# Optimization experiments

Hardware: AMD Instinct MI355X
Metric: run time of the kernel (lower is better)

The kernel has to match this reference:

```python
import jax, jax.numpy as jnp
import numpy as np

B, S, RAW, E, H, NH = 2048, 8, 1024, 512, 256, 8
CEIL = 0.9998


def _lstm_dir(x, Wih, Whh, bih, bhh, reverse):
    # x: [B,S,D] -> hs: [B,S,H]; torch gate order i,f,g,o
    xs = jnp.swapaxes(x, 0, 1)  # [S,B,D]
    if reverse:
        xs = xs[::-1]
    pre = jnp.einsum('sbd,gd->sbg', xs, Wih) + bih + bhh  # [S,B,4H]
    h0 = jnp.zeros((x.shape[0], Whh.shape[1]), x.dtype)

    def step(carry, p):
        h, c = carry
        g = p + h @ Whh.T
        i, f, gg, o = jnp.split(g, 4, axis=-1)
        c = jax.nn.sigmoid(f) * c + jax.nn.sigmoid(i) * jnp.tanh(gg)
        h = jax.nn.sigmoid(o) * jnp.tanh(c)
        return (h, c), h

    _, hs = jax.lax.scan(step, (h0, h0), pre)
    if reverse:
        hs = hs[::-1]
    return jnp.swapaxes(hs, 0, 1)


def _bilstm(x, Wih, Whh, bih, bhh):
    # stacked weights: Wih [2,2,4H,512], Whh [2,2,4H,H], biases [2,2,4H]
    for l in range(2):
        fwd = _lstm_dir(x, Wih[l, 0], Whh[l, 0], bih[l, 0], bhh[l, 0], False)
        bwd = _lstm_dir(x, Wih[l, 1], Whh[l, 1], bih[l, 1], bhh[l, 1], True)
        x = jnp.concatenate([fwd, bwd], axis=-1)  # [B,S,2H]
    return x


def _mha(x, Wqkv, bqkv, Wo, bo):
    b, s, e = x.shape
    hd = e // NH
    qkv = x @ Wqkv.T + bqkv
    q, k, v = jnp.split(qkv, 3, axis=-1)
    q = q.reshape(b, s, NH, hd).transpose(0, 2, 1, 3)
    k = k.reshape(b, s, NH, hd).transpose(0, 2, 1, 3)
    v = v.reshape(b, s, NH, hd).transpose(0, 2, 1, 3)
    attn = jax.nn.softmax(jnp.einsum('bhqd,bhkd->bhqk', q, k) / jnp.sqrt(jnp.float32(hd)), axis=-1)
    out = jnp.einsum('bhqk,bhkd->bhqd', attn, v).transpose(0, 2, 1, 3).reshape(b, s, e)
    out = out @ Wo.T + bo
    return out, attn.mean(axis=1)  # torch averages weights over heads -> [B,S,S]


def _mlp2(x, W1, b1, W2, b2):
    return jax.nn.relu(x @ W1.T + b1) @ W2.T + b2


def setup_inputs() -> dict:
    key = jax.random.key(0)
    ks = jax.random.split(key, 32)
    g = lambda k, shp: (0.02 * jax.random.normal(k, shp)).astype(jnp.float32)
    inp = {
        'audio_raw': jax.random.normal(ks[0], (B, S, RAW), jnp.float32),
        'visual_raw': jax.random.normal(ks[1], (B, S, RAW), jnp.float32),
        'Wa1': g(ks[2], (512, 1024)), 'ba1': g(ks[3], (512,)),
        'Wa2': g(ks[4], (256, 512)), 'ba2': g(ks[5], (256,)),
        'Wv1': g(ks[6], (512, 1024)), 'bv1': g(ks[7], (512,)),
        'Wv2': g(ks[8], (256, 512)), 'bv2': g(ks[9], (256,)),
        'Wih': g(ks[10], (2, 2, 4 * H, 512)), 'Whh': g(ks[11], (2, 2, 4 * H, H)),
        'bih': g(ks[12], (2, 2, 4 * H)), 'bhh': g(ks[13], (2, 2, 4 * H)),
        'Wqkv': g(ks[14], (3 * E, E)), 'bqkv': g(ks[15], (3 * E,)),
        'Wo': g(ks[16], (E, E)), 'bo': g(ks[17], (E,)),
        'Wc1': g(ks[18], (256, E + 1)), 'bc1': g(ks[19], (256,)),
        'Wc2': g(ks[20], (1, 256)), 'bc2': g(ks[21], (1,)),
    }
    return inp


def reference(audio_raw, visual_raw, Wa1, ba1, Wa2, ba2, Wv1, bv1, Wv2, bv2,
              Wih, Whh, bih, bhh, Wqkv, bqkv, Wo, bo, Wc1, bc1, Wc2, bc2):
    a = _mlp2(audio_raw, Wa1, ba1, Wa2, ba2)    # [B,S,256]
    v = _mlp2(visual_raw, Wv1, bv1, Wv2, bv2)   # [B,S,256]
    seq = jnp.concatenate([a, v], axis=-1)      # [B,S,512]
    lstm_out = _bilstm(seq, Wih, Whh, bih, bhh)  # [B,S,512]
    attn_out, attn_w = _mha(lstm_out, Wqkv, bqkv, Wo, bo)
    weights = jax.nn.softmax(attn_w.mean(axis=1), axis=-1)          # [B,S]
    summary = jnp.einsum('bse,bs->be', attn_out, weights)           # [B,512]
    curiosity_bonus = jnp.zeros((summary.shape[0], 1), summary.dtype)  # replay buffer empty
    c_in = jnp.concatenate([summary, curiosity_bonus], axis=-1)
    coherence = jax.nn.sigmoid(jax.nn.relu(c_in @ Wc1.T + bc1) @ Wc2.T + bc2)[:, 0]
    coherence = jnp.minimum(coherence, CEIL)  # absolute-ceiling veto clip
    return coherence
```

## Files before the change

### kernel.cpp

```cpp
#include <hip/hip_runtime.h>
#include <hip/hip_bf16.h>


#define ROWS   16384
#define BATCH  2048

typedef __bf16 bf16x8 __attribute__((ext_vector_type(8)));
typedef float  f32x4  __attribute__((ext_vector_type(4)));

typedef __hip_bfloat16 bf16;

#define MB(x) ((size_t)(x) << 20)
static const size_t OFF_WB    = 0;
static const size_t OFF_ABF   = MB(12);
static const size_t OFF_VBF   = MB(44);
static const size_t OFF_M1A   = MB(76);
static const size_t OFF_M1V   = MB(92);
static const size_t OFF_SEQ   = MB(108);
static const size_t OFF_PRE   = MB(124);
static const size_t OFF_LSTM1 = MB(210);
static const size_t OFF_LSTM2 = MB(226);
static const size_t OFF_QKV   = MB(12);
static const size_t OFF_CTX   = MB(108);
static const size_t OFF_AOUT  = MB(12);
static const size_t OFF_COLSUM= MB(242);
static const size_t OFF_WTS   = MB(243);
static const size_t OFF_SUMM  = MB(244);
static const size_t OFF_WC1T  = MB(248);

static const size_t WB_WA1  = 0;
static const size_t WB_WV1  = 524288;
static const size_t WB_WA2  = 1048576;
static const size_t WB_WV2  = 1179648;
static const size_t WB_WIH  = 1310720;
static const size_t WB_WHH  = 3407872;
static const size_t WB_WQKV = 4456448;
static const size_t WB_WO   = 5242880;

struct ConvJobs {
    const float* src[10];
    bf16*        dst[10];
    long long    cum[11];
};

__global__ __launch_bounds__(256) void convert_bf16(ConvJobs jobs, long long total4)
{
    for (long long g = (long long)blockIdx.x * 256 + threadIdx.x; g < total4;
         g += (long long)gridDim.x * 256) {
        int j = 0;
        while (g >= jobs.cum[j + 1]) ++j;
        const long long idx = g - jobs.cum[j];
        const float4 v = ((const float4*)jobs.src[j])[idx];
        union { ushort4 u; bf16 h[4]; } p;
        p.h[0] = __float2bfloat16(v.x);
        p.h[1] = __float2bfloat16(v.y);
        p.h[2] = __float2bfloat16(v.z);
        p.h[3] = __float2bfloat16(v.w);
        ((ushort4*)jobs.dst[j])[idx] = p.u;
    }
}

__device__ __forceinline__ void gload_lds16(const void* g, void* l)
{
    __builtin_amdgcn_global_load_lds(
        (const __attribute__((address_space(1))) unsigned int*)g,
        (__attribute__((address_space(3))) unsigned int*)l, 16, 0, 0);
}

__global__ __launch_bounds__(256) void gemm_mfma(
    const bf16* __restrict__ A, long long sAz,
    const bf16* __restrict__ W, long long sWz,
    const float* __restrict__ b1, long long sb1,
    const float* __restrict__ b2, long long sb2,
    const bf16* __restrict__ D, long long sDz, int ldd,
    float* Cf, long long sCfz,
    bf16* Cb, long long sCbz,
    int M, int N, int K, int ldc, int coloff, int relu)
{
    const int z = blockIdx.z;
    A += (long long)z * sAz;
    W += (long long)z * sWz;
    if (b1) b1 += (long long)z * sb1;
    if (b2) b2 += (long long)z * sb2;
    if (D)  D  += (long long)z * sDz;
    if (Cf) Cf += (long long)z * sCfz;
    if (Cb) Cb += (long long)z * sCbz;

    __shared__ bf16 As[128 * 32];
    __shared__ bf16 Bs[128 * 32];

    const int tid  = threadIdx.x;
    const int wave = tid >> 6;
    const int lane = tid & 63;
    const int wm = wave >> 1;
    const int wn = wave & 1;
    const long long m0 = (long long)blockIdx.x * 128;
    const long long n0 = (long long)blockIdx.y * 128;

    const int srow = tid >> 2;
    const int scol = (tid & 3) * 8;

    f32x4 acc[4][4] = {};

    const bf16* Abase = A + (m0 + srow) * (long long)K + scol;
    const bf16* Wbase = W + (n0 + srow) * (long long)K + scol;
    const long long K64 = (long long)K * 64;

    const int lrow = (lane >> 4) * 8;
    const int frow = lane & 15;

    for (int k0 = 0; k0 < K; k0 += 32) {
        gload_lds16(Abase + k0,        As + tid * 8);
        gload_lds16(Abase + k0 + K64,  As + 2048 + tid * 8);
        gload_lds16(Wbase + k0,        Bs + tid * 8);
        gload_lds16(Wbase + k0 + K64,  Bs + 2048 + tid * 8);
        __syncthreads();

        bf16x8 af[4], bfv[4];
#pragma unroll
        for (int i = 0; i < 4; ++i)
            af[i] = *(const bf16x8*)(As + (wm * 64 + i * 16 + frow) * 32 + lrow);
#pragma unroll
        for (int j = 0; j < 4; ++j)
            bfv[j] = *(const bf16x8*)(Bs + (wn * 64 + j * 16 + frow) * 32 + lrow);
#pragma unroll
        for (int i = 0; i < 4; ++i)
#pragma unroll
            for (int j = 0; j < 4; ++j)
                acc[i][j] = __builtin_amdgcn_mfma_f32_16x16x32_bf16(af[i], bfv[j], acc[i][j], 0, 0, 0);
        __syncthreads();
    }

    const long long mwb = m0 + wm * 64;
    const long long nwb = n0 + wn * 64;
    const int rbase = (lane >> 4) * 4;
    const int lcol = lane & 15;
#pragma unroll
    for (int j = 0; j < 4; ++j) {
        const long long col = nwb + j * 16 + lcol;
        float bias = 0.f;
        if (b1) bias += b1[col];
        if (b2) bias += b2[col];
#pragma unroll
        for (int i = 0; i < 4; ++i) {
            const long long rowb = mwb + i * 16 + rbase;
#pragma unroll
            for (int r = 0; r < 4; ++r) {
                const long long row = rowb + r;
                float v = acc[i][j][r] + bias;
                if (D) v += __bfloat162float(D[row * (long long)ldd + col]);
                if (relu) v = fmaxf(v, 0.f);
                if (Cf) Cf[row * (long long)ldc + coloff + col] = v;
                if (Cb) Cb[row * (long long)ldc + coloff + col] = __float2bfloat16(v);
            }
        }
    }
}

__device__ __forceinline__ float sigf(float x) { return 1.f / (1.f + expf(-x)); }

__global__ __launch_bounds__(512) void lstm_layer(
    const bf16* __restrict__ PRE,
    const bf16* __restrict__ Whh,
    bf16* __restrict__ lout)
{
    __shared__ bf16 Bs[128 * 256];
    __shared__ bf16 Hs[16 * 264];

    float* preact = (float*)Bs;

    const int tid  = threadIdx.x;
    const int wave = tid >> 6;
    const int lane = tid & 63;
    const int frow = lane & 15;
    const int g    = lane >> 4;
    const int rbase = g * 4;

    const int R0  = blockIdx.x * 16;
    const int dir = R0 >> 11;
    const int b0  = R0 & 2047;
    const bf16* Wd   = Whh + (size_t)dir * 1024 * 256;
    const bf16* PREd = PRE + (size_t)dir * 16384 * 1024;

    const int gn = tid & 255;
    const int rh = tid >> 8;

    float c_state[8];
#pragma unroll
    for (int i = 0; i < 8; ++i) c_state[i] = 0.f;

    for (int t = 0; t < 8; ++t) {
        if (t > 0) {
            bf16x8 af[8];
#pragma unroll
            for (int ks = 0; ks < 8; ++ks)
                af[ks] = *(const bf16x8*)(Hs + frow * 264 + ks * 32 + g * 8);

            f32x4 acc[8] = {};
            for (int nb = 0; nb < 8; ++nb) {
                __syncthreads();
                const bf16* src = Wd + (size_t)nb * 128 * 256;
#pragma unroll
                for (int q = 0; q < 8; ++q) {
                    const int t16 = q * 512 + tid;
                    const int row = t16 >> 5;
                    const int cl  = t16 & 31;
                    const int cg  = cl ^ (row & 7);
                    gload_lds16(src + row * 256 + cg * 8, Bs + t16 * 8);
                }
                __syncthreads();
                const int lr = wave * 16 + frow;
#pragma unroll
                for (int ks = 0; ks < 8; ++ks) {
                    const int cgk = ks * 4 + g;
                    const bf16x8 bv = *(const bf16x8*)(Bs + lr * 256 + ((cgk ^ (lr & 7)) * 8));
                    acc[nb] = __builtin_amdgcn_mfma_f32_16x16x32_bf16(af[ks], bv, acc[nb], 0, 0, 0);
                }
            }
            __syncthreads();
#pragma unroll
            for (int nb = 0; nb < 8; ++nb) {
                const int col = nb * 128 + wave * 16 + frow;
#pragma unroll
                for (int r = 0; r < 4; ++r)
                    preact[(rbase + r) * 1024 + col] = acc[nb][r];
            }
            __syncthreads();
        }

        const int te = dir ? (7 - t) : t;
#pragma unroll
        for (int i = 0; i < 8; ++i) {
            const int row = i * 2 + rh;
            const int b = b0 + row;
            const bf16* pr = PREd + ((size_t)b * 8 + te) * 1024;
            float ig = __bfloat162float(pr[gn]);
            float fg = __bfloat162float(pr[gn + 256]);
            float gg = __bfloat162float(pr[gn + 512]);
            float og = __bfloat162float(pr[gn + 768]);
            if (t > 0) {
                ig += preact[row * 1024 + gn];
                fg += preact[row * 1024 + gn + 256];
                gg += preact[row * 1024 + gn + 512];
                og += preact[row * 1024 + gn + 768];
            }
            const float c = sigf(fg) * c_state[i] + sigf(ig) * tanhf(gg);
            const float h = sigf(og) * tanhf(c);
            c_state[i] = c;
            Hs[row * 264 + gn] = __float2bfloat16(h);
            lout[((size_t)b * 8 + te) * 512 + dir * 256 + gn] = __float2bfloat16(h);
        }
        __syncthreads();
    }
}

__global__ __launch_bounds__(64) void attn_kernel(
    const bf16* __restrict__ qkv,
    bf16* __restrict__ ctx,
    float* __restrict__ colsum)
{
    const int bh = blockIdx.x;
    const int b = bh >> 3;
    const int h = bh & 7;
    const int t = threadIdx.x;

    __shared__ float q[8][64], k[8][64], v[8][64], p[8][8];
    const bf16* base = qkv + (size_t)b * 8 * 1536 + h * 64;
#pragma unroll
    for (int s = 0; s < 8; ++s) {
        q[s][t] = __bfloat162float(base[s * 1536 + t]);
        k[s][t] = __bfloat162float(base[s * 1536 + 512 + t]);
        v[s][t] = __bfloat162float(base[s * 1536 + 1024 + t]);
    }
    __syncthreads();

    const int qi = t >> 3;
    const int kj = t & 7;
    float sc = 0.f;
#pragma unroll
    for (int d = 0; d < 64; ++d) sc += q[qi][d] * k[kj][d];
    sc *= 0.125f;

    float mx = sc;
    for (int off = 1; off < 8; off <<= 1) mx = fmaxf(mx, __shfl_xor(mx, off));
    const float e = expf(sc - mx);
    float sum = e;
    for (int off = 1; off < 8; off <<= 1) sum += __shfl_xor(sum, off);
    const float P = e / sum;
    p[qi][kj] = P;

    float cs = P;
    for (int off = 8; off < 64; off <<= 1) cs += __shfl_xor(cs, off);
    if (t < 8) colsum[(size_t)bh * 8 + t] = cs;
    __syncthreads();

    bf16* cb = ctx + ((size_t)b * 8 + qi) * 512 + h * 64;
#pragma unroll
    for (int j = 0; j < 8; ++j) {
        const int d = (t & 7) + 8 * j;
        float o = 0.f;
#pragma unroll
        for (int kk = 0; kk < 8; ++kk) o += p[qi][kk] * v[kk][d];
        cb[d] = __float2bfloat16(o);
    }
}

__global__ __launch_bounds__(64) void weights_kernel(
    const float* __restrict__ colsum, float* __restrict__ wts)
{
    const int t = threadIdx.x;
    const int b = blockIdx.x * 8 + (t >> 3);
    const int kk = t & 7;
    const float* cs = colsum + (size_t)b * 64;
    float s = 0.f;
#pragma unroll
    for (int h = 0; h < 8; ++h) s += cs[h * 8 + kk];
    s *= (1.f / 64.f);
    float mx = s;
    for (int off = 1; off < 8; off <<= 1) mx = fmaxf(mx, __shfl_xor(mx, off));
    const float e = expf(s - mx);
    float sum = e;
    for (int off = 1; off < 8; off <<= 1) sum += __shfl_xor(sum, off);
    wts[(size_t)b * 8 + kk] = e / sum;
}

__global__ __launch_bounds__(256) void summary_kernel(
    const float* __restrict__ aout, const float* __restrict__ wts,
    float* __restrict__ summ)
{
    const int gid = blockIdx.x * 256 + threadIdx.x;
    const int b = gid >> 9;
    const int e = gid & 511;
    const float* ab = aout + (size_t)b * 8 * 512 + e;
    const float* wb = wts + (size_t)b * 8;
    float s = 0.f;
#pragma unroll
    for (int t = 0; t < 8; ++t) s += ab[t * 512] * wb[t];
    summ[gid] = s;
}

__global__ __launch_bounds__(256) void transpose_wc1(
    const float* __restrict__ Wc1, float* __restrict__ Wc1T)
{
    const int gid = blockIdx.x * 256 + threadIdx.x;
    const int j = gid / 513;
    const int e = gid % 513;
    Wc1T[(size_t)e * 256 + j] = Wc1[gid];
}

__global__ __launch_bounds__(256) void coherence_kernel(
    const float* __restrict__ summ, const float* __restrict__ Wc1T,
    const float* __restrict__ bc1, const float* __restrict__ Wc2,
    const float* __restrict__ bc2, float* __restrict__ out)
{
    const int b = blockIdx.x;
    const int j = threadIdx.x;
    __shared__ float s[512];
    __shared__ float red[4];
    s[j]       = summ[(size_t)b * 512 + j];
    s[j + 256] = summ[(size_t)b * 512 + 256 + j];
    __syncthreads();

    float hj = bc1[j];
    for (int e = 0; e < 512; ++e) hj += s[e] * Wc1T[(size_t)e * 256 + j];
    hj = fmaxf(hj, 0.f);
    float val = hj * Wc2[j];
    for (int off = 1; off < 64; off <<= 1) val += __shfl_xor(val, off);
    if ((j & 63) == 0) red[j >> 6] = val;
    __syncthreads();
    if (j == 0) {
        const float tot = red[0] + red[1] + red[2] + red[3] + bc2[0];
        const float c = 1.f / (1.f + expf(-tot));
        out[b] = fminf(c, 0.9998f);
    }
}

extern "C" void kernel_launch(void* const* d_in, const int* in_sizes, int n_in,
                              void* d_out, int out_size, void* d_ws, size_t ws_size,
                              hipStream_t stream)
{
    (void)in_sizes; (void)n_in; (void)out_size; (void)ws_size;

    const float* audio  = (const float*)d_in[0];
    const float* visual = (const float*)d_in[1];
    const float* Wa1 = (const float*)d_in[2];  const float* ba1 = (const float*)d_in[3];
    const float* Wa2 = (const float*)d_in[4];  const float* ba2 = (const float*)d_in[5];
    const float* Wv1 = (const float*)d_in[6];  const float* bv1 = (const float*)d_in[7];
    const float* Wv2 = (const float*)d_in[8];  const float* bv2 = (const float*)d_in[9];
    const float* Wih = (const float*)d_in[10]; const float* Whh = (const float*)d_in[11];
    const float* bih = (const float*)d_in[12]; const float* bhh = (const float*)d_in[13];
    const float* Wqkv = (const float*)d_in[14]; const float* bqkv = (const float*)d_in[15];
    const float* Wo  = (const float*)d_in[16]; const float* bo  = (const float*)d_in[17];
    const float* Wc1 = (const float*)d_in[18]; const float* bc1 = (const float*)d_in[19];
    const float* Wc2 = (const float*)d_in[20]; const float* bc2 = (const float*)d_in[21];

    char* wsb = (char*)d_ws;
    float* out = (float*)d_out;

    bf16* WB    = (bf16*)(wsb + OFF_WB);
    bf16* ABF   = (bf16*)(wsb + OFF_ABF);
    bf16* VBF   = (bf16*)(wsb + OFF_VBF);
    bf16* M1A   = (bf16*)(wsb + OFF_M1A);
    bf16* M1V   = (bf16*)(wsb + OFF_M1V);
    bf16* SEQ   = (bf16*)(wsb + OFF_SEQ);
    bf16* PRE   = (bf16*)(wsb + OFF_PRE);
    bf16* LSTM1 = (bf16*)(wsb + OFF_LSTM1);
    bf16* LSTM2 = (bf16*)(wsb + OFF_LSTM2);
    bf16* QKVB  = (bf16*)(wsb + OFF_QKV);
    bf16* CTX   = (bf16*)(wsb + OFF_CTX);
    float* AOUT = (float*)(wsb + OFF_AOUT);
    float* COLSUM = (float*)(wsb + OFF_COLSUM);
    float* WTS  = (float*)(wsb + OFF_WTS);
    float* SUMM = (float*)(wsb + OFF_SUMM);
    float* WC1T = (float*)(wsb + OFF_WC1T);

    bf16* Wa1b = WB + WB_WA1;  bf16* Wv1b = WB + WB_WV1;
    bf16* Wa2b = WB + WB_WA2;  bf16* Wv2b = WB + WB_WV2;
    bf16* Wihb = WB + WB_WIH;  bf16* Whhb = WB + WB_WHH;
    bf16* Wqkvb = WB + WB_WQKV; bf16* Wob = WB + WB_WO;

    {
        ConvJobs cj;
        const float* srcs[10] = {audio, visual, Wa1, Wa2, Wv1, Wv2, Wih, Whh, Wqkv, Wo};
        bf16* dsts[10] = {ABF, VBF, Wa1b, Wa2b, Wv1b, Wv2b, Wihb, Whhb, Wqkvb, Wob};
        const long long cnt4[10] = {4194304, 4194304, 131072, 32768, 131072, 32768,
                                    524288, 262144, 196608, 65536};
        long long cum = 0;
        for (int i = 0; i < 10; ++i) {
            cj.src[i] = srcs[i]; cj.dst[i] = dsts[i];
            cj.cum[i] = cum; cum += cnt4[i];
        }
        cj.cum[10] = cum;
        hipLaunchKernelGGL(convert_bf16, dim3(2048), dim3(256), 0, stream, cj, cum);
    }

    auto gemm = [&](const bf16* A, long long sAz, const bf16* W, long long sWz,
                    const float* b1, long long sb1, const float* b2, long long sb2,
                    const bf16* D, long long sDz, int ldd,
                    float* Cf, long long sCfz, bf16* Cb, long long sCbz,
                    int M, int N, int K, int ldc, int coloff, int relu, int nz) {
        dim3 grid(M / 128, N / 128, nz);
        hipLaunchKernelGGL(gemm_mfma, grid, dim3(256), 0, stream,
                           A, sAz, W, sWz, b1, sb1, b2, sb2, D, sDz, ldd,
                           Cf, sCfz, Cb, sCbz, M, N, K, ldc, coloff, relu);
    };

    gemm(ABF, 0, Wa1b, 0, ba1, 0, nullptr, 0, nullptr, 0, 0,
         nullptr, 0, M1A, 0, ROWS, 512, 1024, 512, 0, 1, 1);
    gemm(VBF, 0, Wv1b, 0, bv1, 0, nullptr, 0, nullptr, 0, 0,
         nullptr, 0, M1V, 0, ROWS, 512, 1024, 512, 0, 1, 1);
    gemm(M1A, 0, Wa2b, 0, ba2, 0, nullptr, 0, nullptr, 0, 0,
         nullptr, 0, SEQ, 0, ROWS, 256, 512, 512, 0, 0, 1);
    gemm(M1V, 0, Wv2b, 0, bv2, 0, nullptr, 0, nullptr, 0, 0,
         nullptr, 0, SEQ, 0, ROWS, 256, 512, 512, 256, 0, 1);

    for (int l = 0; l < 2; ++l) {
        const bf16* xin = (l == 0) ? SEQ : LSTM1;
        bf16* lout      = (l == 0) ? LSTM1 : LSTM2;
        const bf16* Wih_l = Wihb + (size_t)l * 2 * 1024 * 512;
        const bf16* Whh_l = Whhb + (size_t)l * 2 * 1024 * 256;
        const float* bih_l = bih + (size_t)l * 2 * 1024;
        const float* bhh_l = bhh + (size_t)l * 2 * 1024;

        gemm(xin, 0, Wih_l, 1024LL * 512, bih_l, 1024, bhh_l, 1024,
             nullptr, 0, 0, nullptr, 0, PRE, 16384LL * 1024,
             ROWS, 1024, 512, 1024, 0, 0, 2);

        hipLaunchKernelGGL(lstm_layer, dim3(256), dim3(512), 0, stream,
                           PRE, Whh_l, lout);
    }

    gemm(LSTM2, 0, Wqkvb, 0, bqkv, 0, nullptr, 0, nullptr, 0, 0,
         nullptr, 0, QKVB, 0, ROWS, 1536, 512, 1536, 0, 0, 1);
    hipLaunchKernelGGL(attn_kernel, dim3(BATCH * 8), dim3(64), 0, stream, QKVB, CTX, COLSUM);
    hipLaunchKernelGGL(weights_kernel, dim3(BATCH / 8), dim3(64), 0, stream, COLSUM, WTS);
    gemm(CTX, 0, Wob, 0, bo, 0, nullptr, 0, nullptr, 0, 0,
         AOUT, 0, nullptr, 0, ROWS, 512, 512, 512, 0, 0, 1);

    hipLaunchKernelGGL(summary_kernel, dim3(BATCH * 512 / 256), dim3(256), 0, stream,
                       AOUT, WTS, SUMM);
    hipLaunchKernelGGL(transpose_wc1, dim3(513), dim3(256), 0, stream, Wc1, WC1T);
    hipLaunchKernelGGL(coherence_kernel, dim3(BATCH), dim3(256), 0, stream,
                       SUMM, WC1T, bc1, Wc2, bc2, out);
}
```

Measured before the change: 813.2 us.

## Double-buffer Whh tiles and keep LSTM gate math in registers

The LSTM recurrent kernel now double-buffers the Whh weight chunks in LDS. Loads for chunk c+2 are issued while chunk c is consumed, using explicit vmcnt waits and raw barriers in place of full syncthreads. The gate-to-column mapping is rearranged so each wave accumulates all four gates for the same hidden units in registers. This removes the round trip of preactivations through shared memory, and the input preactivations are prefetched before the matmul. The LDS footprint doubles and the hand-written waitcnt/barrier sequencing is fragile. Only half the waves do MFMA work on each chunk.

```diff
diff --git a/kernel.cpp b/kernel.cpp
--- a/kernel.cpp
+++ b/kernel.cpp
@@ -159,22 +159,19 @@
 
 __device__ __forceinline__ float sigf(float x) { return 1.f / (1.f + expf(-x)); }
 
-__global__ __launch_bounds__(512) void lstm_layer(
+__global__ __launch_bounds__(512, 2) void lstm_layer(
     const bf16* __restrict__ PRE,
     const bf16* __restrict__ Whh,
     bf16* __restrict__ lout)
 {
-    __shared__ bf16 Bs[128 * 256];
+    __shared__ bf16 Bs[2][128 * 256];
     __shared__ bf16 Hs[16 * 264];
-
-    float* preact = (float*)Bs;
 
     const int tid  = threadIdx.x;
     const int wave = tid >> 6;
     const int lane = tid & 63;
     const int frow = lane & 15;
-    const int g    = lane >> 4;
-    const int rbase = g * 4;
+    const int g8   = lane >> 4;
 
     const int R0  = blockIdx.x * 16;
     const int dir = R0 >> 11;
@@ -182,76 +179,90 @@
     const bf16* Wd   = Whh + (size_t)dir * 1024 * 256;
     const bf16* PREd = PRE + (size_t)dir * 16384 * 1024;
 
-    const int gn = tid & 255;
-    const int rh = tid >> 8;
-
-    float c_state[8];
-#pragma unroll
-    for (int i = 0; i < 8; ++i) c_state[i] = 0.f;
+    float cst[2][4] = {};
+
+#define STAGE(c, bi)                                                        \
+    {                                                                       \
+        const bf16* _src = Wd + (size_t)(c) * 128 * 256;                    \
+        _Pragma("unroll")                                                   \
+        for (int _q = 0; _q < 8; ++_q) {                                    \
+            const int _t16 = _q * 512 + tid;                                \
+            const int _row = _t16 >> 5;                                     \
+            const int _cg  = (_t16 & 31) ^ (_row & 7);                      \
+            gload_lds16(_src + _row * 256 + _cg * 8, &Bs[bi][_t16 * 8]);    \
+        }                                                                   \
+    }
+
+    STAGE(0, 0);
+    STAGE(1, 1);
 
     for (int t = 0; t < 8; ++t) {
+        const int te = dir ? (7 - t) : t;
+
+        float pv[4][2][4];
+#pragma unroll
+        for (int r = 0; r < 4; ++r) {
+            const bf16* pr = PREd + ((size_t)(b0 + g8 * 4 + r) * 8 + te) * 1024
+                             + wave * 32 + frow;
+#pragma unroll
+            for (int q = 0; q < 4; ++q)
+#pragma unroll
+                for (int nc = 0; nc < 2; ++nc)
+                    pv[q][nc][r] = __bfloat162float(pr[q * 256 + nc * 16]);
+        }
+
+        f32x4 acc[4][2] = {};
         if (t > 0) {
             bf16x8 af[8];
 #pragma unroll
             for (int ks = 0; ks < 8; ++ks)
-                af[ks] = *(const bf16x8*)(Hs + frow * 264 + ks * 32 + g * 8);
-
-            f32x4 acc[8] = {};
-            for (int nb = 0; nb < 8; ++nb) {
-                __syncthreads();
-                const bf16* src = Wd + (size_t)nb * 128 * 256;
-#pragma unroll
-                for (int q = 0; q < 8; ++q) {
-                    const int t16 = q * 512 + tid;
-                    const int row = t16 >> 5;
-                    const int cl  = t16 & 31;
-                    const int cg  = cl ^ (row & 7);
-                    gload_lds16(src + row * 256 + cg * 8, Bs + t16 * 8);
+                af[ks] = *(const bf16x8*)(Hs + frow * 264 + ks * 32 + g8 * 8);
+
+#pragma unroll
+            for (int c = 0; c < 8; ++c) {
+                asm volatile("s_waitcnt vmcnt(8)" ::: "memory");
+                __builtin_amdgcn_s_barrier();
+                if ((wave >> 2) == (c & 1)) {
+                    const int rb = (wave & 3) * 32;
+#pragma unroll
+                    for (int nc = 0; nc < 2; ++nc) {
+                        const int rl = rb + nc * 16 + frow;
+#pragma unroll
+                        for (int ks = 0; ks < 8; ++ks) {
+                            const bf16x8 bv = *(const bf16x8*)(
+                                &Bs[c & 1][rl * 256 + (((ks * 4 + g8) ^ (rl & 7)) * 8)]);
+                            acc[c >> 1][nc] = __builtin_amdgcn_mfma_f32_16x16x32_bf16(
+                                af[ks], bv, acc[c >> 1][nc], 0, 0, 0);
+                        }
+                    }
                 }
-                __syncthreads();
-                const int lr = wave * 16 + frow;
-#pragma unroll
-                for (int ks = 0; ks < 8; ++ks) {
-                    const int cgk = ks * 4 + g;
-                    const bf16x8 bv = *(const bf16x8*)(Bs + lr * 256 + ((cgk ^ (lr & 7)) * 8));
-                    acc[nb] = __builtin_amdgcn_mfma_f32_16x16x32_bf16(af[ks], bv, acc[nb], 0, 0, 0);
-                }
+                asm volatile("s_waitcnt lgkmcnt(0)" ::: "memory");
+                __builtin_amdgcn_s_barrier();
+                if (t < 7 || c < 6) STAGE((c + 2) & 7, c & 1);
             }
-            __syncthreads();
-#pragma unroll
-            for (int nb = 0; nb < 8; ++nb) {
-                const int col = nb * 128 + wave * 16 + frow;
-#pragma unroll
-                for (int r = 0; r < 4; ++r)
-                    preact[(rbase + r) * 1024 + col] = acc[nb][r];
+        }
+
+#pragma unroll
+        for (int nc = 0; nc < 2; ++nc)
+#pragma unroll
+            for (int r = 0; r < 4; ++r) {
+                const float ig = pv[0][nc][r] + acc[0][nc][r];
+                const float fg = pv[1][nc][r] + acc[1][nc][r];
+                const float gg = pv[2][nc][r] + acc[2][nc][r];
+                const float og = pv[3][nc][r] + acc[3][nc][r];
+                const float cc = sigf(fg) * cst[nc][r] + sigf(ig) * tanhf(gg);
+                const float hh = sigf(og) * tanhf(cc);
+                cst[nc][r] = cc;
+                const int row = g8 * 4 + r;
+                const int n   = wave * 32 + nc * 16 + frow;
+                Hs[row * 264 + n] = __float2bfloat16(hh);
+                lout[((size_t)(b0 + row) * 8 + te) * 512 + dir * 256 + n] =
+                    __float2bfloat16(hh);
             }
-            __syncthreads();
-        }
-
-        const int te = dir ? (7 - t) : t;
-#pragma unroll
-        for (int i = 0; i < 8; ++i) {
-            const int row = i * 2 + rh;
-            const int b = b0 + row;
-            const bf16* pr = PREd + ((size_t)b * 8 + te) * 1024;
-            float ig = __bfloat162float(pr[gn]);
-            float fg = __bfloat162float(pr[gn + 256]);
-            float gg = __bfloat162float(pr[gn + 512]);
-            float og = __bfloat162float(pr[gn + 768]);
-            if (t > 0) {
-                ig += preact[row * 1024 + gn];
-                fg += preact[row * 1024 + gn + 256];
-                gg += preact[row * 1024 + gn + 512];
-                og += preact[row * 1024 + gn + 768];
-            }
-            const float c = sigf(fg) * c_state[i] + sigf(ig) * tanhf(gg);
-            const float h = sigf(og) * tanhf(c);
-            c_state[i] = c;
-            Hs[row * 264 + gn] = __float2bfloat16(h);
-            lout[((size_t)b * 8 + te) * 512 + dir * 256 + gn] = __float2bfloat16(h);
-        }
-        __syncthreads();
-    }
+        asm volatile("s_waitcnt lgkmcnt(0)" ::: "memory");
+        __builtin_amdgcn_s_barrier();
+    }
+#undef STAGE
 }
 
 __global__ __launch_bounds__(64) void attn_kernel(
```

Result: slower. 912.2 us (+12.2%).
